# Kernel tuning notes

Measured on AMD Instinct MI355X. Metric: run time of the kernel, lower is better.

The kernel has to match this reference:

```python
import jax, jax.numpy as jnp
import numpy as np

FMAPS = 128
B, F, N = 16, 128, 2048


def setup_inputs() -> dict:
    key = jax.random.key(0)
    k1, k2, k3 = jax.random.split(key, 3)
    adj_in = jnp.zeros((B, N, N), dtype=jnp.float32)  # unused by the math (device-check only in torch)
    emb_in = jax.random.normal(k1, (B, F, N), dtype=jnp.float32)
    # parameters, initialized like torch.rand (uniform [0,1))
    v = jax.random.uniform(k2, (FMAPS,), dtype=jnp.float32)
    b = jax.random.uniform(k3, (1,), dtype=jnp.float32)
    return {"adj_in": adj_in, "emb_in": emb_in, "v": v, "b": b}


def reference(adj_in, emb_in, v, b):
    # coord = emb_in / emb_in.std()  (torch std: unbiased over all elements)
    coord = emb_in / jnp.std(emb_in, ddof=1)
    # adj[b,i,j] = sum_f v[f]*(coord[b,f,i] + coord[b,f,j]) + bias
    # = s[b,i] + s[b,j] + bias, where s = v . coord  -> O(B*F*N) instead of per-node bmm loop
    s = jnp.einsum("f,bfn->bn", v, coord)  # [B, N]
    adj = jax.nn.sigmoid(s[:, :, None] + s[:, None, :] + b[0])  # [B, N, N]
    return adj
```

## Files before the change

### kernel.cpp

```cpp
#include <hip/hip_runtime.h>
#include <hip/hip_bf16.h>

#define B_ 16
#define F_ 128
#define N_ 2048
#define M_TOT (B_ * F_ * N_)

__global__ __launch_bounds__(256) void k_reduce(const float* __restrict__ emb,
                                                float* __restrict__ partials) {
    int tid = threadIdx.x;
    int gid = blockIdx.x * blockDim.x + tid;
    int stride = gridDim.x * blockDim.x;

    float s = 0.f, q = 0.f;
    const float4* e4 = (const float4*)emb;
    const int total4 = M_TOT / 4;
    for (int i = gid; i < total4; i += stride) {
        float4 v = e4[i];
        s += v.x + v.y + v.z + v.w;
        q += v.x * v.x + v.y * v.y + v.z * v.z + v.w * v.w;
    }

    #pragma unroll
    for (int off = 32; off > 0; off >>= 1) {
        s += __shfl_down(s, off);
        q += __shfl_down(q, off);
    }

    __shared__ float ls[4], lq[4];
    int wave = tid >> 6;
    if ((tid & 63) == 0) { ls[wave] = s; lq[wave] = q; }
    __syncthreads();
    if (tid == 0) {
        float S = ls[0] + ls[1] + ls[2] + ls[3];
        float Q = lq[0] + lq[1] + lq[2] + lq[3];
        partials[2 * blockIdx.x]     = S;
        partials[2 * blockIdx.x + 1] = Q;
    }
}

__global__ __launch_bounds__(256) void k_finalize(const float* __restrict__ partials,
                                                  float* __restrict__ inv_std,
                                                  int nblk) {
    int tid = threadIdx.x;
    float s = 0.f, q = 0.f;
    for (int i = tid; i < nblk; i += blockDim.x) {
        s += partials[2 * i];
        q += partials[2 * i + 1];
    }
    #pragma unroll
    for (int off = 32; off > 0; off >>= 1) {
        s += __shfl_down(s, off);
        q += __shfl_down(q, off);
    }
    __shared__ float ls[4], lq[4];
    int wave = tid >> 6;
    if ((tid & 63) == 0) { ls[wave] = s; lq[wave] = q; }
    __syncthreads();
    if (tid == 0) {
        float S = ls[0] + ls[1] + ls[2] + ls[3];
        float Q = lq[0] + lq[1] + lq[2] + lq[3];
        float mean = S / (float)M_TOT;
        float var = (Q - S * mean) / (float)(M_TOT - 1);
        inv_std[0] = rsqrtf(var);
    }
}

__global__ __launch_bounds__(256) void k_dot(const float* __restrict__ emb,
                                             const float* __restrict__ v,
                                             const float* __restrict__ bias,
                                             const float* __restrict__ inv_std,
                                             float* __restrict__ t) {
    __shared__ float vs[F_];
    int tid = threadIdx.x;
    if (tid < F_) vs[tid] = v[tid];
    __syncthreads();

    int idx = blockIdx.x * blockDim.x + tid;
    int b = idx >> 11;
    int n = idx & (N_ - 1);
    const float* base = emb + (size_t)b * F_ * N_ + n;

    float acc = 0.f;
    #pragma unroll 8
    for (int f = 0; f < F_; ++f) {
        acc += vs[f] * base[(size_t)f * N_];
    }
    t[idx] = acc * inv_std[0] + 0.5f * bias[0];
}

__device__ __forceinline__ float fast_sigmoid(float x) {
    float e = __expf(-x);
    return __builtin_amdgcn_rcpf(1.0f + e);
}

__global__ __launch_bounds__(256) void k_out(const float* __restrict__ t,
                                             float* __restrict__ out) {
    int row = blockIdx.x;
    int b = row >> 11;
    float si = t[row];

    const float4* t4 = (const float4*)(t + ((size_t)b << 11));
    float4* o4 = (float4*)(out + (size_t)row * N_);

    int tid = threadIdx.x;
    #pragma unroll
    for (int k = 0; k < 2; ++k) {
        int j4 = tid + k * 256;
        float4 tj = t4[j4];
        float4 r;
        r.x = fast_sigmoid(si + tj.x);
        r.y = fast_sigmoid(si + tj.y);
        r.z = fast_sigmoid(si + tj.z);
        r.w = fast_sigmoid(si + tj.w);
        o4[j4] = r;
    }
}

extern "C" void kernel_launch(void* const* d_in, const int* in_sizes, int n_in,
                              void* d_out, int out_size, void* d_ws, size_t ws_size,
                              hipStream_t stream) {
    const float* emb  = (const float*)d_in[1];
    const float* v    = (const float*)d_in[2];
    const float* bias = (const float*)d_in[3];
    float* out = (float*)d_out;

    float* wsf      = (float*)d_ws;
    float* partials = wsf;
    float* inv_std  = wsf + 2048;
    float* t        = wsf + 2304;

    const int RB = 1024;

    k_reduce<<<RB, 256, 0, stream>>>(emb, partials);
    k_finalize<<<1, 256, 0, stream>>>(partials, inv_std, RB);
    k_dot<<<(B_ * N_) / 256, 256, 0, stream>>>(emb, v, bias, inv_std, t);
    k_out<<<B_ * N_, 256, 0, stream>>>(t, out);
}
```

Before: 397.5 us.

## Fuse std reduction with dot product and process four output rows per block

```diff
diff --git a/kernel.cpp b/kernel.cpp
--- a/kernel.cpp
+++ b/kernel.cpp
@@ -6,48 +6,50 @@
 #define N_ 2048
 #define M_TOT (B_ * F_ * N_)
 
-__global__ __launch_bounds__(256) void k_reduce(const float* __restrict__ emb,
-                                                float* __restrict__ partials) {
+__global__ __launch_bounds__(128) void k_fused(const float* __restrict__ emb,
+                                               const float* __restrict__ v,
+                                               float* __restrict__ d,
+                                               float* __restrict__ partials) {
+    __shared__ float vs[F_];
     int tid = threadIdx.x;
-    int gid = blockIdx.x * blockDim.x + tid;
-    int stride = gridDim.x * blockDim.x;
+    vs[tid] = v[tid];
+    __syncthreads();
 
-    float s = 0.f, q = 0.f;
-    const float4* e4 = (const float4*)emb;
-    const int total4 = M_TOT / 4;
-    for (int i = gid; i < total4; i += stride) {
-        float4 v = e4[i];
-        s += v.x + v.y + v.z + v.w;
-        q += v.x * v.x + v.y * v.y + v.z * v.z + v.w * v.w;
+    int col = blockIdx.x * 128 + tid;
+    int b = col >> 11;
+    int n = col & (N_ - 1);
+    const float* base = emb + (size_t)b * F_ * N_ + n;
+
+    float acc = 0.f, s = 0.f, q = 0.f;
+    #pragma unroll 16
+    for (int f = 0; f < F_; ++f) {
+        float x = base[(size_t)f * N_];
+        acc += vs[f] * x;
+        s += x;
+        q += x * x;
     }
+    d[col] = acc;
 
     #pragma unroll
     for (int off = 32; off > 0; off >>= 1) {
         s += __shfl_down(s, off);
         q += __shfl_down(q, off);
     }
-
-    __shared__ float ls[4], lq[4];
+    __shared__ float ls[2], lq[2];
     int wave = tid >> 6;
     if ((tid & 63) == 0) { ls[wave] = s; lq[wave] = q; }
     __syncthreads();
     if (tid == 0) {
-        float S = ls[0] + ls[1] + ls[2] + ls[3];
-        float Q = lq[0] + lq[1] + lq[2] + lq[3];
-        partials[2 * blockIdx.x]     = S;
-        partials[2 * blockIdx.x + 1] = Q;
+        partials[2 * blockIdx.x]     = ls[0] + ls[1];
+        partials[2 * blockIdx.x + 1] = lq[0] + lq[1];
     }
 }
 
 __global__ __launch_bounds__(256) void k_finalize(const float* __restrict__ partials,
-                                                  float* __restrict__ inv_std,
-                                                  int nblk) {
+                                                  float* __restrict__ inv_std) {
     int tid = threadIdx.x;
-    float s = 0.f, q = 0.f;
-    for (int i = tid; i < nblk; i += blockDim.x) {
-        s += partials[2 * i];
-        q += partials[2 * i + 1];
-    }
+    float s = partials[2 * tid];
+    float q = partials[2 * tid + 1];
     #pragma unroll
     for (int off = 32; off > 0; off >>= 1) {
         s += __shfl_down(s, off);
@@ -66,54 +68,51 @@
     }
 }
 
-__global__ __launch_bounds__(256) void k_dot(const float* __restrict__ emb,
-                                             const float* __restrict__ v,
-                                             const float* __restrict__ bias,
-                                             const float* __restrict__ inv_std,
-                                             float* __restrict__ t) {
-    __shared__ float vs[F_];
-    int tid = threadIdx.x;
-    if (tid < F_) vs[tid] = v[tid];
-    __syncthreads();
-
-    int idx = blockIdx.x * blockDim.x + tid;
-    int b = idx >> 11;
-    int n = idx & (N_ - 1);
-    const float* base = emb + (size_t)b * F_ * N_ + n;
-
-    float acc = 0.f;
-    #pragma unroll 8
-    for (int f = 0; f < F_; ++f) {
-        acc += vs[f] * base[(size_t)f * N_];
-    }
-    t[idx] = acc * inv_std[0] + 0.5f * bias[0];
-}
-
 __device__ __forceinline__ float fast_sigmoid(float x) {
     float e = __expf(-x);
     return __builtin_amdgcn_rcpf(1.0f + e);
 }
 
-__global__ __launch_bounds__(256) void k_out(const float* __restrict__ t,
+__global__ __launch_bounds__(256) void k_out(const float* __restrict__ d,
+                                             const float* __restrict__ inv_std_p,
+                                             const float* __restrict__ bias,
                                              float* __restrict__ out) {
-    int row = blockIdx.x;
-    int b = row >> 11;
-    float si = t[row];
+    __shared__ float tjs[N_];
+    int blk = blockIdx.x;
+    int b  = blk >> 9;
+    int i0 = (blk & 511) * 4;
+    int tid = threadIdx.x;
 
-    const float4* t4 = (const float4*)(t + ((size_t)b << 11));
-    float4* o4 = (float4*)(out + (size_t)row * N_);
+    float is = inv_std_p[0];
+    float bb = bias[0];
+    const float* db = d + ((size_t)b << 11);
 
-    int tid = threadIdx.x;
     #pragma unroll
-    for (int k = 0; k < 2; ++k) {
-        int j4 = tid + k * 256;
-        float4 tj = t4[j4];
-        float4 r;
-        r.x = fast_sigmoid(si + tj.x);
-        r.y = fast_sigmoid(si + tj.y);
-        r.z = fast_sigmoid(si + tj.z);
-        r.w = fast_sigmoid(si + tj.w);
-        o4[j4] = r;
+    for (int k = 0; k < 8; ++k) {
+        int j = tid + k * 256;
+        tjs[j] = is * db[j];
+    }
+    __syncthreads();
+
+    float a[4];
+    #pragma unroll
+    for (int r = 0; r < 4; ++r) a[r] = tjs[i0 + r] + bb;
+
+    float4* o4 = (float4*)(out + ((size_t)b * N_ + i0) * N_);
+
+    #pragma unroll
+    for (int r = 0; r < 4; ++r) {
+        #pragma unroll
+        for (int k = 0; k < 2; ++k) {
+            int j4 = tid + k * 256;
+            float4 tj = *(const float4*)&tjs[j4 * 4];
+            float4 rr;
+            rr.x = fast_sigmoid(a[r] + tj.x);
+            rr.y = fast_sigmoid(a[r] + tj.y);
+            rr.z = fast_sigmoid(a[r] + tj.z);
+            rr.w = fast_sigmoid(a[r] + tj.w);
+            o4[(size_t)r * 512 + j4] = rr;
+        }
     }
 }
 
@@ -126,14 +125,11 @@
     float* out = (float*)d_out;
 
     float* wsf      = (float*)d_ws;
-    float* partials = wsf;
-    float* inv_std  = wsf + 2048;
-    float* t        = wsf + 2304;
+    float* d        = wsf;
+    float* partials = wsf + 32768;
+    float* inv_std  = wsf + 32768 + 512;
 
-    const int RB = 1024;
-
-    k_reduce<<<RB, 256, 0, stream>>>(emb, partials);
-    k_finalize<<<1, 256, 0, stream>>>(partials, inv_std, RB);
-    k_dot<<<(B_ * N_) / 256, 256, 0, stream>>>(emb, v, bias, inv_std, t);
-    k_out<<<B_ * N_, 256, 0, stream>>>(t, out);
+    k_fused<<<256, 128, 0, stream>>>(emb, v, d, partials);
+    k_finalize<<<1, 256, 0, stream>>>(partials, inv_std);
+    k_out<<<8192, 256, 0, stream>>>(d, inv_std, bias, out);
 }
```

After: 400.8 us. About the same (+0.8%).
